# Kernel tuning notes

Measured on AMD Instinct MI355X. Metric: run time of the kernel, lower is better.

## Reference

```python
import jax, jax.numpy as jnp
import numpy as np

N = 8192
IN_F = 512
OUT_F = 64
ALPHA = 0.2  # LeakyReLU negative slope
NEG_INF = -9e15


def setup_inputs() -> dict:
    key = jax.random.key(0)
    k1, k2, k3, k4 = jax.random.split(key, 4)
    x = jax.random.normal(k1, (N, IN_F), dtype=jnp.float32)
    adj = jax.random.randint(k2, (N, N), 0, 2, dtype=jnp.int32)
    # xavier_uniform with gain=1.414
    def xavier(k, shape, gain=1.414):
        fan_in, fan_out = shape[0], shape[1]
        a = gain * np.sqrt(6.0 / (fan_in + fan_out))
        return jax.random.uniform(k, shape, jnp.float32, -a, a)
    W = xavier(k3, (IN_F, OUT_F))
    a = xavier(k4, (2 * OUT_F, 1))
    return {"x": x, "adj": adj, "W": W, "a": a}


def reference(x, adj, W, a):
    h = x @ W  # [N, F]
    f = W.shape[1]
    # e[i,j] = leakyrelu([h_i, h_j] @ a) = leakyrelu(h_i@a1 + h_j@a2)
    e1 = h @ a[:f, 0]   # [N]
    e2 = h @ a[f:, 0]   # [N]
    e = jax.nn.leaky_relu(e1[:, None] + e2[None, :], negative_slope=ALPHA)  # [N, N]
    scores = jnp.where(adj > 0, e, NEG_INF)
    attention = jax.nn.softmax(scores, axis=1)  # dropout p=0.0 -> identity
    h_prime = attention @ h  # [N, F]
    return jax.nn.elu(h_prime)  # concat=True
```

## Files before the change

kernel.cpp:

```cpp
#include <hip/hip_runtime.h>
#include <hip/hip_bf16.h>

#define NN 8192
#define KF 512
#define FF 64
#define GAT_ALPHA 0.2f
#define MSHIFT 20.0f
#define LOG2E 1.44269504f

#define JSPLIT 8
#define JW (NN / JSPLIT)
#define NSUB 4
#define SUBJ 256
#define SUBK 8
#define HTS 264

#define EXP2F(x) __builtin_amdgcn_exp2f(x)

typedef __attribute__((ext_vector_type(8))) __bf16 bf16x8;
typedef __attribute__((ext_vector_type(4))) float f32x4;
typedef __attribute__((ext_vector_type(4))) int   i32x4;

__device__ __forceinline__ unsigned pack_bf16_rne(float hi, float lo) {
    unsigned uh = __float_as_uint(hi);
    unsigned ul = __float_as_uint(lo);
    uh = uh + 0x7FFFu + ((uh >> 16) & 1u);
    ul = ul + 0x7FFFu + ((ul >> 16) & 1u);
    return (uh & 0xFFFF0000u) | (ul >> 16);
}

__global__ __launch_bounds__(256) void gat_linear(
    const float* __restrict__ x, const float* __restrict__ W,
    const float* __restrict__ av, __hip_bfloat16* __restrict__ ht,
    float* __restrict__ e1, float* __restrict__ e2)
{
    __shared__ float xs[32][33];
    __shared__ float Ws[32][64];
    __shared__ float ep[2][32][17];

    const int t  = threadIdx.x;
    const int fq = t & 15;
    const int rq = t >> 4;
    const int i0 = blockIdx.x * 32;

    const int kl = t & 31, r0 = t >> 5;
    const int fw = t & 63, kq = t >> 6;

    float acc[2][4] = {};

    for (int kt = 0; kt < KF; kt += 32) {
        #pragma unroll
        for (int m = 0; m < 4; ++m)
            xs[kl][r0 + 8 * m] = x[(size_t)(i0 + r0 + 8 * m) * KF + kt + kl];
        #pragma unroll
        for (int m = 0; m < 8; ++m)
            Ws[kq + 4 * m][fw] = W[(size_t)(kt + kq + 4 * m) * FF + fw];
        __syncthreads();
        #pragma unroll
        for (int kk = 0; kk < 32; ++kk) {
            float x0 = xs[kk][rq * 2];
            float x1 = xs[kk][rq * 2 + 1];
            f32x4 wv = *(const f32x4*)&Ws[kk][fq * 4];
            #pragma unroll
            for (int v = 0; v < 4; ++v) {
                acc[0][v] += x0 * wv[v];
                acc[1][v] += x1 * wv[v];
            }
        }
        __syncthreads();
    }

    #pragma unroll
    for (int v = 0; v < 4; ++v) {
        int f = fq * 4 + v;
        unsigned w = pack_bf16_rne(acc[1][v], acc[0][v]);
        *(unsigned*)&ht[(size_t)f * NN + i0 + rq * 2] = w;
    }

    f32x4 a1v = *(const f32x4*)&av[fq * 4];
    f32x4 a2v = *(const f32x4*)&av[64 + fq * 4];
    #pragma unroll
    for (int u = 0; u < 2; ++u) {
        float s1 = 0.f, s2 = 0.f;
        #pragma unroll
        for (int v = 0; v < 4; ++v) {
            s1 += acc[u][v] * a1v[v];
            s2 += acc[u][v] * a2v[v];
        }
        ep[0][rq * 2 + u][fq] = s1;
        ep[1][rq * 2 + u][fq] = s2;
    }
    __syncthreads();
    if (t < 32) {
        float s1 = 0.f, s2 = 0.f;
        #pragma unroll
        for (int q = 0; q < 16; ++q) { s1 += ep[0][t][q]; s2 += ep[1][t][q]; }
        e1[i0 + t] = s1 * LOG2E;
        e2[i0 + t] = s2 * LOG2E;
    }
}

__global__ __launch_bounds__(256) void gat_attn(
    const int* __restrict__ adj, const __hip_bfloat16* __restrict__ ht,
    const float* __restrict__ e1, const float* __restrict__ e2,
    float* __restrict__ accs, float* __restrict__ lsums)
{
    __shared__ __hip_bfloat16 hs[2][64 * HTS];
    __shared__ unsigned msk32[64 * 33];
    __shared__ float e2s[JW];

    const int t     = threadIdx.x;
    const int lane  = t & 63;
    const int wv    = t >> 6;
    const int n16   = lane & 15;
    const int quad  = lane >> 4;
    const int split = blockIdx.x & (JSPLIT - 1);
    const int i0b   = (blockIdx.x >> 3) * 64;
    const int i0    = i0b + wv * 16;
    const int j0    = split * JW;
    const int rowl  = wv * 16 + n16;
    const int row   = i0 + n16;

    {
        const int stt = t & 31;
        const int rr  = t >> 5;
        #pragma unroll
        for (int rep = 0; rep < 8; ++rep) {
            const int r = rep * 8 + rr;
            const int* ap = adj + (size_t)(i0b + r) * NN + j0 + stt * 32;
            unsigned w = 0;
            #pragma unroll
            for (int k = 0; k < 8; ++k) {
                int4 v = *(const int4*)(ap + k * 4);
                unsigned nib =  (unsigned)(v.x > 0)
                             | ((unsigned)(v.y > 0) << 1)
                             | ((unsigned)(v.z > 0) << 2)
                             | ((unsigned)(v.w > 0) << 3);
                w |= nib << (k * 4);
            }
            msk32[r * 33 + stt] = w;
        }
    }
    *(float4*)&e2s[t * 4] = *(const float4*)&e2[j0 + t * 4];
    #pragma unroll
    for (int c = 0; c < 8; ++c) {
        int g = t + c * 256, f = g >> 5, jl = (g & 31) * 8;
        *(bf16x8*)&hs[0][f * HTS + jl] = *(const bf16x8*)&ht[(size_t)f * NN + j0 + jl];
    }
    __syncthreads();

    const float e1L = e1[row];
    float ms = e1L + MSHIFT * LOG2E;
    const float miL = ms > 0.f ? ms : GAT_ALPHA * ms;
    const float c0  = e1L - miL;
    const float c1  = GAT_ALPHA * e1L - miL;

    const float* ep0 = e2s + quad * 8;

    f32x4 dacc0 = {0.f,0.f,0.f,0.f}, dacc1 = {0.f,0.f,0.f,0.f};
    f32x4 dacc2 = {0.f,0.f,0.f,0.f}, dacc3 = {0.f,0.f,0.f,0.f};
    f32x4 dl    = {0.f,0.f,0.f,0.f};

    const i32x4 ones_i = {0x3F803F80, 0x3F803F80, 0x3F803F80, 0x3F803F80};
    const bf16x8 ones  = __builtin_bit_cast(bf16x8, ones_i);

    for (int sub = 0; sub < NSUB; ++sub) {
        const int buf = sub & 1;

        bf16x8 hreg[8];
        if (sub + 1 < NSUB) {
            #pragma unroll
            for (int c = 0; c < 8; ++c) {
                int g = t + c * 256, f = g >> 5, jl = (g & 31) * 8;
                hreg[c] = *(const bf16x8*)&ht[(size_t)f * NN + j0 + (sub + 1) * SUBJ + jl];
            }
        }

        #pragma unroll
        for (int k = 0; k < SUBK; ++k) {
            const int stg = sub * SUBK + k;
            unsigned mw = msk32[rowl * 33 + stg];
            unsigned mc = mw >> (quad * 8);
            f32x4 e0 = *(const f32x4*)(ep0 + stg * 32);
            f32x4 ev = *(const f32x4*)(ep0 + stg * 32 + 4);
            const __hip_bfloat16* hb = &hs[buf][n16 * HTS + k * 32 + quad * 8];
            bf16x8 b0 = *(const bf16x8*)(hb);
            bf16x8 b1 = *(const bf16x8*)(hb + 16 * HTS);
            bf16x8 b2 = *(const bf16x8*)(hb + 32 * HTS);
            bf16x8 b3 = *(const bf16x8*)(hb + 48 * HTS);

#define PJ(eval, bit)                                                          \
            ( ((mc >> (bit)) & 1u)                                             \
                ? EXP2F(fmaxf(c0 + (eval), __builtin_fmaf(GAT_ALPHA, (eval), c1))) \
                : 0.f )
            float p0 = PJ(e0.x, 0);
            float p1 = PJ(e0.y, 1);
            float p2 = PJ(e0.z, 2);
            float p3 = PJ(e0.w, 3);
            float p4 = PJ(ev.x, 4);
            float p5 = PJ(ev.y, 5);
            float p6 = PJ(ev.z, 6);
            float p7 = PJ(ev.w, 7);
#undef PJ
            i32x4 iv;
            iv.x = (int)pack_bf16_rne(p1, p0);
            iv.y = (int)pack_bf16_rne(p3, p2);
            iv.z = (int)pack_bf16_rne(p5, p4);
            iv.w = (int)pack_bf16_rne(p7, p6);
            bf16x8 af = __builtin_bit_cast(bf16x8, iv);

            dacc0 = __builtin_amdgcn_mfma_f32_16x16x32_bf16(af, b0, dacc0, 0, 0, 0);
            dacc1 = __builtin_amdgcn_mfma_f32_16x16x32_bf16(af, b1, dacc1, 0, 0, 0);
            dacc2 = __builtin_amdgcn_mfma_f32_16x16x32_bf16(af, b2, dacc2, 0, 0, 0);
            dacc3 = __builtin_amdgcn_mfma_f32_16x16x32_bf16(af, b3, dacc3, 0, 0, 0);
            dl    = __builtin_amdgcn_mfma_f32_16x16x32_bf16(af, ones, dl, 0, 0, 0);
        }

        if (sub + 1 < NSUB) {
            #pragma unroll
            for (int c = 0; c < 8; ++c) {
                int g = t + c * 256, f = g >> 5, jl = (g & 31) * 8;
                *(bf16x8*)&hs[buf ^ 1][f * HTS + jl] = hreg[c];
            }
        }
        __syncthreads();
    }

    if (n16 == 0) {
        lsums[(size_t)split * NN + i0 + quad * 4 + 0] = dl.x;
        lsums[(size_t)split * NN + i0 + quad * 4 + 1] = dl.y;
        lsums[(size_t)split * NN + i0 + quad * 4 + 2] = dl.z;
        lsums[(size_t)split * NN + i0 + quad * 4 + 3] = dl.w;
    }

    float* ab = accs + (size_t)split * NN * FF + (size_t)(i0 + quad * 4) * FF + n16;
#define STORE4(dv, ftofs)                                                      \
    ab[0 * FF + (ftofs)] = (dv).x;                                             \
    ab[1 * FF + (ftofs)] = (dv).y;                                             \
    ab[2 * FF + (ftofs)] = (dv).z;                                             \
    ab[3 * FF + (ftofs)] = (dv).w;
    STORE4(dacc0, 0)
    STORE4(dacc1, 16)
    STORE4(dacc2, 32)
    STORE4(dacc3, 48)
#undef STORE4
}

__global__ __launch_bounds__(256) void gat_epilogue(
    const float* __restrict__ accs, const float* __restrict__ lsums,
    float* __restrict__ out)
{
    const int idx = (blockIdx.x * 256 + threadIdx.x) * 4;
    const int row = idx >> 6;

    float l = 0.f;
    #pragma unroll
    for (int s = 0; s < JSPLIT; ++s) l += lsums[(size_t)s * NN + row];

    f32x4 a = {0.f, 0.f, 0.f, 0.f};
    #pragma unroll
    for (int s = 0; s < JSPLIT; ++s) {
        f32x4 v = *(const f32x4*)(accs + (size_t)s * NN * FF + idx);
        a.x += v.x; a.y += v.y; a.z += v.z; a.w += v.w;
    }

    const float li = 1.f / l;
    f32x4 o;
    o.x = a.x * li; o.y = a.y * li; o.z = a.z * li; o.w = a.w * li;
    o.x = o.x > 0.f ? o.x : __expf(o.x) - 1.f;
    o.y = o.y > 0.f ? o.y : __expf(o.y) - 1.f;
    o.z = o.z > 0.f ? o.z : __expf(o.z) - 1.f;
    o.w = o.w > 0.f ? o.w : __expf(o.w) - 1.f;
    *(f32x4*)(out + idx) = o;
}

extern "C" void kernel_launch(void* const* d_in, const int* in_sizes, int n_in,
                              void* d_out, int out_size, void* d_ws, size_t ws_size,
                              hipStream_t stream) {
    const float* x   = (const float*)d_in[0];
    const int*   adj = (const int*)d_in[1];
    const float* W   = (const float*)d_in[2];
    const float* av  = (const float*)d_in[3];
    float* out = (float*)d_out;

    char* wsb = (char*)d_ws;
    __hip_bfloat16* ht = (__hip_bfloat16*)wsb;
    float* e1    = (float*)(wsb + (1 << 20));
    float* e2    = e1 + NN;
    float* accs  = e2 + NN;
    float* lsums = accs + (size_t)JSPLIT * NN * FF;

    gat_linear<<<256, 256, 0, stream>>>(x, W, av, ht, e1, e2);
    gat_attn<<<(NN / 64) * JSPLIT, 256, 0, stream>>>(adj, ht, e1, e2, accs, lsums);
    gat_epilogue<<<NN * FF / 1024, 256, 0, stream>>>(accs, lsums, out);
}
```

Before: 416.3 us.

## Double JSPLIT and single-buffer h tile to raise attention kernel occupancy

Splits the neighbour dimension into 16 chunks instead of 8, so each block covers 512 columns and the grid doubles. The double-buffered h tile and register prefetch are replaced by one LDS buffer loaded in two synchronous phases, which cuts LDS use and register pressure. Launch bounds now request 4 blocks per SM. The cost is that global loads no longer overlap with MFMA work inside a block, and twice as many partial accumulators must be written and reduced.

```diff
diff --git a/kernel.cpp b/kernel.cpp
--- a/kernel.cpp
+++ b/kernel.cpp
@@ -8,11 +8,10 @@
 #define MSHIFT 20.0f
 #define LOG2E 1.44269504f
 
-#define JSPLIT 8
+#define JSPLIT 16
 #define JW (NN / JSPLIT)
-#define NSUB 4
-#define SUBJ 256
-#define SUBK 8
+#define KSTEPS 16
+#define PSTEP 8
 #define HTS 264
 
 #define EXP2F(x) __builtin_amdgcn_exp2f(x)
@@ -100,13 +99,13 @@
     }
 }
 
-__global__ __launch_bounds__(256) void gat_attn(
+__global__ __launch_bounds__(256, 4) void gat_attn(
     const int* __restrict__ adj, const __hip_bfloat16* __restrict__ ht,
     const float* __restrict__ e1, const float* __restrict__ e2,
     float* __restrict__ accs, float* __restrict__ lsums)
 {
-    __shared__ __hip_bfloat16 hs[2][64 * HTS];
-    __shared__ unsigned msk32[64 * 33];
+    __shared__ __hip_bfloat16 hs[64 * HTS];
+    __shared__ unsigned msk32[64 * 17];
     __shared__ float e2s[JW];
 
     const int t     = threadIdx.x;
@@ -115,18 +114,18 @@
     const int n16   = lane & 15;
     const int quad  = lane >> 4;
     const int split = blockIdx.x & (JSPLIT - 1);
-    const int i0b   = (blockIdx.x >> 3) * 64;
+    const int i0b   = (blockIdx.x >> 4) * 64;
     const int i0    = i0b + wv * 16;
     const int j0    = split * JW;
     const int rowl  = wv * 16 + n16;
     const int row   = i0 + n16;
 
     {
-        const int stt = t & 31;
-        const int rr  = t >> 5;
-        #pragma unroll
-        for (int rep = 0; rep < 8; ++rep) {
-            const int r = rep * 8 + rr;
+        const int stt = t & 15;
+        const int rr  = t >> 4;
+        #pragma unroll
+        for (int rep = 0; rep < 4; ++rep) {
+            const int r = rep * 16 + rr;
             const int* ap = adj + (size_t)(i0b + r) * NN + j0 + stt * 32;
             unsigned w = 0;
             #pragma unroll
@@ -138,16 +137,11 @@
                              | ((unsigned)(v.w > 0) << 3);
                 w |= nib << (k * 4);
             }
-            msk32[r * 33 + stt] = w;
-        }
-    }
-    *(float4*)&e2s[t * 4] = *(const float4*)&e2[j0 + t * 4];
-    #pragma unroll
-    for (int c = 0; c < 8; ++c) {
-        int g = t + c * 256, f = g >> 5, jl = (g & 31) * 8;
-        *(bf16x8*)&hs[0][f * HTS + jl] = *(const bf16x8*)&ht[(size_t)f * NN + j0 + jl];
-    }
-    __syncthreads();
+            msk32[r * 17 + stt] = w;
+        }
+    }
+    if (t < JW / 4)
+        *(float4*)&e2s[t * 4] = *(const float4*)&e2[j0 + t * 4];
 
     const float e1L = e1[row];
     float ms = e1L + MSHIFT * LOG2E;
@@ -164,26 +158,24 @@
     const i32x4 ones_i = {0x3F803F80, 0x3F803F80, 0x3F803F80, 0x3F803F80};
     const bf16x8 ones  = __builtin_bit_cast(bf16x8, ones_i);
 
-    for (int sub = 0; sub < NSUB; ++sub) {
-        const int buf = sub & 1;
-
-        bf16x8 hreg[8];
-        if (sub + 1 < NSUB) {
-            #pragma unroll
-            for (int c = 0; c < 8; ++c) {
-                int g = t + c * 256, f = g >> 5, jl = (g & 31) * 8;
-                hreg[c] = *(const bf16x8*)&ht[(size_t)f * NN + j0 + (sub + 1) * SUBJ + jl];
-            }
-        }
-
-        #pragma unroll
-        for (int k = 0; k < SUBK; ++k) {
-            const int stg = sub * SUBK + k;
-            unsigned mw = msk32[rowl * 33 + stg];
+    #pragma unroll
+    for (int ph = 0; ph < 2; ++ph) {
+        #pragma unroll
+        for (int c = 0; c < 8; ++c) {
+            int g = t + c * 256, f = g >> 5, jl = (g & 31) * 8;
+            *(bf16x8*)&hs[f * HTS + jl] =
+                *(const bf16x8*)&ht[(size_t)f * NN + j0 + ph * 256 + jl];
+        }
+        __syncthreads();
+
+        #pragma unroll
+        for (int k = 0; k < PSTEP; ++k) {
+            const int stg = ph * PSTEP + k;
+            unsigned mw = msk32[rowl * 17 + stg];
             unsigned mc = mw >> (quad * 8);
             f32x4 e0 = *(const f32x4*)(ep0 + stg * 32);
             f32x4 ev = *(const f32x4*)(ep0 + stg * 32 + 4);
-            const __hip_bfloat16* hb = &hs[buf][n16 * HTS + k * 32 + quad * 8];
+            const __hip_bfloat16* hb = &hs[n16 * HTS + k * 32 + quad * 8];
             bf16x8 b0 = *(const bf16x8*)(hb);
             bf16x8 b1 = *(const bf16x8*)(hb + 16 * HTS);
             bf16x8 b2 = *(const bf16x8*)(hb + 32 * HTS);
@@ -215,15 +207,7 @@
             dacc3 = __builtin_amdgcn_mfma_f32_16x16x32_bf16(af, b3, dacc3, 0, 0, 0);
             dl    = __builtin_amdgcn_mfma_f32_16x16x32_bf16(af, ones, dl, 0, 0, 0);
         }
-
-        if (sub + 1 < NSUB) {
-            #pragma unroll
-            for (int c = 0; c < 8; ++c) {
-                int g = t + c * 256, f = g >> 5, jl = (g & 31) * 8;
-                *(bf16x8*)&hs[buf ^ 1][f * HTS + jl] = hreg[c];
-            }
-        }
-        __syncthreads();
+        if (ph == 0) __syncthreads();
     }
 
     if (n16 == 0) {
```

After: 403.8 us. -3.0%, faster.
